# Optimization experiments

Measured on AMD Instinct MI355X. Metric: run time of the kernel, lower is better.

The kernel has to match this reference:

```python
import jax, jax.numpy as jnp
import numpy as np

H = 96
W = 96
FX = 96.0
FY = 96.0
NEAR = 0.3
EPS = 1e-8


def q2r(quat):
    # quat: [N,4] (w,x,y,z) -> [N,3,3]
    q = quat / (jnp.linalg.norm(quat, axis=-1, keepdims=True) + 1e-12)
    w, x, y, z = q[:, 0], q[:, 1], q[:, 2], q[:, 3]
    R = jnp.stack([
        1 - 2 * (y * y + z * z), 2 * (x * y - w * z), 2 * (x * z + w * y),
        2 * (x * y + w * z), 1 - 2 * (x * x + z * z), 2 * (y * z - w * x),
        2 * (x * z - w * y), 2 * (y * z + w * x), 1 - 2 * (x * x + y * y),
    ], axis=-1).reshape(-1, 3, 3)
    return R


def setup_inputs() -> dict:
    key = jax.random.key(0)
    ks = jax.random.split(key, 8)
    N = 4096
    pos_xy = jax.random.uniform(ks[0], (N, 2), minval=-2.0, maxval=2.0, dtype=jnp.float32)
    pos_z = jax.random.uniform(ks[1], (N, 1), minval=2.0, maxval=6.0, dtype=jnp.float32)
    pos = jnp.concatenate([pos_xy, pos_z], axis=-1)
    rgb = jax.random.normal(ks[2], (N, 3), dtype=jnp.float32)
    opa = jax.random.normal(ks[3], (N,), dtype=jnp.float32)
    quat = jax.random.normal(ks[4], (N, 4), dtype=jnp.float32)
    scale = jax.random.uniform(ks[5], (N, 3), dtype=jnp.float32) * 0.05 + 0.005
    rot = jnp.eye(3, dtype=jnp.float32)
    tran = jnp.zeros(3, dtype=jnp.float32)
    return {"pos": pos, "rgb": rgb, "opa": opa, "quat": quat, "scale": scale, "rot": rot, "tran": tran}


def reference(pos, rgb, opa, quat, scale, rot, tran):
    # ---- project: world -> camera -> image space ----
    cam = pos @ rot.T + tran[None, :]              # [N,3]
    x, y, z = cam[:, 0], cam[:, 1], cam[:, 2]
    r = jnp.linalg.norm(cam, axis=-1)              # depth = ray length (camera_to_image)
    mean2d = jnp.stack([x / z, y / z], axis=-1)    # [N,2]

    # jacobian of (x/z, y/z, |p|) wrt camera-space point, [N,3,3]
    zeros = jnp.zeros_like(z)
    J = jnp.stack([
        1.0 / z, zeros, -x / (z * z),
        zeros, 1.0 / z, -y / (z * z),
        x / r, y / r, z / r,
    ], axis=-1).reshape(-1, 3, 3)

    # ---- 3D covariance: R S S^T R^T ----
    R = q2r(quat)                                   # [N,3,3]
    s = jnp.abs(scale) + 1e-4                       # [N,3]
    RS = R * s[:, None, :]                          # R @ diag(s)
    cov3d = jnp.einsum('nij,nkj->nik', RS, RS)      # [N,3,3]

    # ---- 2D covariance: (J W) cov3d (J W)^T, upper-left 2x2 ----
    JW = jnp.einsum('nij,jk->nik', J, rot)          # [N,3,3]
    cov2d = jnp.einsum('nij,njk,nlk->nil', JW, cov3d, JW)[:, :2, :2]  # [N,2,2]

    a = cov2d[:, 0, 0] + EPS
    d = cov2d[:, 1, 1] + EPS
    b = 0.5 * (cov2d[:, 0, 1] + cov2d[:, 1, 0])
    det = a * d - b * b
    inv_a = d / det
    inv_b = -b / det
    inv_d = a / det

    rgb_act = jax.nn.sigmoid(rgb)                   # [N,3]
    opa_act = jax.nn.sigmoid(opa)                   # [N]

    # ---- per-pixel gaussian evaluation in normalized image space ----
    u = (jnp.arange(W, dtype=jnp.float32) + 0.5 - W / 2) / FX   # [W]
    v = (jnp.arange(H, dtype=jnp.float32) + 0.5 - H / 2) / FY   # [H]
    pu = jnp.tile(u, H)                                          # [P]
    pv = jnp.repeat(v, W)                                        # [P]

    dx = pu[None, :] - mean2d[:, 0:1]               # [N,P]
    dy = pv[None, :] - mean2d[:, 1:2]               # [N,P]
    power = -0.5 * (inv_a[:, None] * dx * dx + 2.0 * inv_b[:, None] * dx * dy + inv_d[:, None] * dy * dy)
    alpha = opa_act[:, None] * jnp.exp(power)       # [N,P]
    alpha = jnp.clip(alpha, 0.0, 0.99)
    valid = (z > NEAR).astype(alpha.dtype)[:, None]
    alpha = alpha * valid

    # ---- depth-sorted alpha compositing ----
    order = jnp.argsort(r)                          # near -> far
    alpha_s = alpha[order]                          # [N,P]
    rgb_s = rgb_act[order]                          # [N,3]

    log_1m = jnp.log1p(-alpha_s)                    # [N,P]
    cum = jnp.cumsum(log_1m, axis=0)
    logT = jnp.concatenate([jnp.zeros((1, alpha_s.shape[1]), alpha_s.dtype), cum[:-1]], axis=0)
    w = jnp.exp(logT) * alpha_s                     # [N,P] blending weights
    img = jnp.einsum('np,nc->pc', w, rgb_s)         # [P,3]
    return img.reshape(H, W, 3)
```

## Files before the change

kernel.cpp:

```cpp
#include <hip/hip_runtime.h>
#include <math.h>

#define N_G   4096
#define IMW   96
#define TILE  6
#define TILES_X 16
#define NTILE (TILES_X*TILES_X)
#define NTHR  1024
#define NW    (NTHR/64)
#define NST   (N_G/NTHR)
#define NPX   (TILE*TILE)
#define NSEG  16
#define BCAP  2048
#define CAP   512
#define FXI   (1.0f/96.0f)
#define NEARP 0.3f
#define EPSV  1e-8f
#define LOG2E 1.4426950408889634f
#define LN2   0.6931471805599453f
#define CULL_K 26.0f

typedef unsigned long long ull;

__global__ __launch_bounds__(NTHR, 1) void splat_k(
    const float* __restrict__ pos, const float* __restrict__ rgb,
    const float* __restrict__ opa, const float* __restrict__ quat,
    const float* __restrict__ scale, const float* __restrict__ rot,
    const float* __restrict__ tran, float* __restrict__ out)
{
    __shared__ unsigned int bl[BCAP];
    __shared__ ull skey[CAP];
    __shared__ float4 g0[CAP], g1[CAP], g2[CAP];
    __shared__ float4 pix[NSEG*NPX];
    __shared__ int wsA[NST][NW];
    __shared__ int wsB[NW];

    const int t = threadIdx.x;
    const int tile = blockIdx.x;
    const int tx = tile % TILES_X, ty = tile / TILES_X;
    const float u0 = ((float)(tx*TILE) + 0.5f - 48.0f) * FXI;
    const float u1 = u0 + (TILE-1) * FXI;
    const float v0 = ((float)(ty*TILE) + 0.5f - 48.0f) * FXI;
    const float v1 = v0 + (TILE-1) * FXI;
    const int wid = t >> 6, lane = t & 63;

    float R00=rot[0],R01=rot[1],R02=rot[2];
    float R10=rot[3],R11=rot[4],R12=rot[5];
    float R20=rot[6],R21=rot[7],R22=rot[8];
    float t0=tran[0], t1=tran[1], t2=tran[2];

    float pp0[NST], pp1[NST], pp2[NST], po[NST], ps0[NST], ps1[NST], ps2[NST];
    #pragma unroll
    for (int st = 0; st < NST; st++) {
        int gi = st*NTHR + t;
        pp0[st]=pos[gi*3+0]; pp1[st]=pos[gi*3+1]; pp2[st]=pos[gi*3+2];
        po[st]=opa[gi];
        ps0[st]=scale[gi*3+0]; ps1[st]=scale[gi*3+1]; ps2[st]=scale[gi*3+2];
    }

    int bcnt = 0;
    #pragma unroll
    for (int st = 0; st < NST; st++) {
        int gi = st*NTHR + t;
        float x = R00*pp0[st] + R01*pp1[st] + R02*pp2[st] + t0;
        float y = R10*pp0[st] + R11*pp1[st] + R12*pp2[st] + t1;
        float z = R20*pp0[st] + R21*pp1[st] + R22*pp2[st] + t2;
        float invz = 1.0f/z;
        float mu = x*invz, mv = y*invz;

        float inz2 = invz*invz;
        float fn = 2.0f*inz2 + (x*x + y*y)*inz2*inz2;
        float smax = fmaxf(fmaxf(fabsf(ps0[st]), fabsf(ps1[st])), fabsf(ps2[st])) + 1e-4f;
        float lmax = fn*smax*smax + EPSV;
        float amp = CULL_K + 1.0f + fminf(0.0f, po[st]*LOG2E);
        float r2b = amp * lmax * (2.0f*LN2) * 1.02f;

        float cu = fminf(fmaxf(mu, u0), u1);
        float cv = fminf(fmaxf(mv, v0), v1);
        float ddx = mu - cu, ddy = mv - cv;
        bool flag = (z > NEARP) && (amp > 0.0f) && (ddx*ddx + ddy*ddy <= r2b);

        ull m = __ballot(flag);
        if (lane == 0) wsA[st][wid] = __popcll(m);
        __syncthreads();
        int base = bcnt, tot = 0;
        #pragma unroll
        for (int w = 0; w < NW; w++) { int c = wsA[st][w]; if (w < wid) base += c; tot += c; }
        if (flag) {
            int p = base + __popcll(m & ((1ull << lane) - 1ull));
            if (p < BCAP) bl[p] = (unsigned int)gi;
        }
        bcnt += tot;
    }
    if (bcnt > BCAP) bcnt = BCAP;
    __syncthreads();

    int cnt = 0;
    for (int s0i = 0; s0i < bcnt; s0i += NTHR) {
        int s = s0i + t;
        bool flag = false;
        float4 o0, o1, o2; float rr = 0.0f;
        if (s < bcnt) {
            int gi = bl[s];
            float p0=pos[gi*3+0], p1=pos[gi*3+1], p2=pos[gi*3+2];
            float x = R00*p0 + R01*p1 + R02*p2 + t0;
            float y = R10*p0 + R11*p1 + R12*p2 + t1;
            float z = R20*p0 + R21*p1 + R22*p2 + t2;
            rr = sqrtf(x*x + y*y + z*z);
            float invz = 1.0f/z;
            float mu = x*invz, mv = y*invz;

            float J02 = -x*invz*invz, J12 = -y*invz*invz;
            float JW00 = invz*R00 + J02*R20;
            float JW01 = invz*R01 + J02*R21;
            float JW02 = invz*R02 + J02*R22;
            float JW10 = invz*R10 + J12*R20;
            float JW11 = invz*R11 + J12*R21;
            float JW12 = invz*R12 + J12*R22;

            float qw=quat[gi*4+0], qx=quat[gi*4+1], qy=quat[gi*4+2], qz=quat[gi*4+3];
            float qn = sqrtf(qw*qw+qx*qx+qy*qy+qz*qz) + 1e-12f;
            float qi = 1.0f/qn;
            qw*=qi; qx*=qi; qy*=qi; qz*=qi;
            float Q00=1.f-2.f*(qy*qy+qz*qz), Q01=2.f*(qx*qy-qw*qz), Q02=2.f*(qx*qz+qw*qy);
            float Q10=2.f*(qx*qy+qw*qz), Q11=1.f-2.f*(qx*qx+qz*qz), Q12=2.f*(qy*qz-qw*qx);
            float Q20=2.f*(qx*qz-qw*qy), Q21=2.f*(qy*qz+qw*qx), Q22=1.f-2.f*(qx*qx+qy*qy);

            float sa=fabsf(scale[gi*3+0])+1e-4f;
            float sb=fabsf(scale[gi*3+1])+1e-4f;
            float sc=fabsf(scale[gi*3+2])+1e-4f;
            float A00=Q00*sa,A01=Q01*sb,A02=Q02*sc;
            float A10=Q10*sa,A11=Q11*sb,A12=Q12*sc;
            float A20=Q20*sa,A21=Q21*sb,A22=Q22*sc;
            float C00=A00*A00+A01*A01+A02*A02;
            float C01=A00*A10+A01*A11+A02*A12;
            float C02=A00*A20+A01*A21+A02*A22;
            float C11=A10*A10+A11*A11+A12*A12;
            float C12=A10*A20+A11*A21+A12*A22;
            float C22=A20*A20+A21*A21+A22*A22;
            float M00=JW00*C00+JW01*C01+JW02*C02;
            float M01=JW00*C01+JW01*C11+JW02*C12;
            float M02=JW00*C02+JW01*C12+JW02*C22;
            float M10=JW10*C00+JW11*C01+JW12*C02;
            float M11=JW10*C01+JW11*C11+JW12*C12;
            float M12=JW10*C02+JW11*C12+JW12*C22;
            float a  = M00*JW00+M01*JW01+M02*JW02 + EPSV;
            float d  = M10*JW10+M11*JW11+M12*JW12 + EPSV;
            float bb = 0.5f*((M00*JW10+M01*JW11+M02*JW12)+(M10*JW00+M11*JW01+M12*JW02));
            float invdet = 1.0f/(a*d - bb*bb);
            float iaP = -0.5f*d*invdet*LOG2E;
            float ibP =  bb*invdet*LOG2E;
            float idP = -0.5f*a*invdet*LOG2E;

            float sig_o = 1.0f/(1.0f+__expf(-opa[gi]));
            float opa_eff = (z > NEARP) ? sig_o : 0.0f;

            float q00 = -iaP, q01 = -0.5f*ibP, q11 = -idP;
            float df = q00 - q11;
            float lam = 0.5f*((q00 + q11) - sqrtf(df*df + 4.0f*q01*q01));
            lam = fmaxf(lam, 1e-20f);
            float r2 = (CULL_K + log2f(opa_eff)) / lam;

            float cu = fminf(fmaxf(mu, u0), u1);
            float cv = fminf(fmaxf(mv, v0), v1);
            float ddx = mu - cu, ddy = mv - cv;
            flag = (ddx*ddx + ddy*ddy) <= r2;

            if (flag) {
                float c0 = 1.0f/(1.0f+__expf(-rgb[gi*3+0]));
                float c1 = 1.0f/(1.0f+__expf(-rgb[gi*3+1]));
                float c2 = 1.0f/(1.0f+__expf(-rgb[gi*3+2]));
                o0 = make_float4(mu, mv, iaP, ibP);
                o1 = make_float4(idP, opa_eff, c0, c1);
                o2 = make_float4(c2, 0.0f, 0.0f, 0.0f);
            }
        }
        ull m = __ballot(flag);
        if (lane == 0) wsB[wid] = __popcll(m);
        __syncthreads();
        int base = cnt, tot = 0;
        #pragma unroll
        for (int w = 0; w < NW; w++) { int c = wsB[w]; if (w < wid) base += c; tot += c; }
        if (flag) {
            int p = base + __popcll(m & ((1ull << lane) - 1ull));
            if (p < CAP) {
                g0[p] = o0; g1[p] = o1; g2[p] = o2;
                skey[p] = ((ull)__float_as_uint(rr) << 32) | (unsigned int)p;
            }
        }
        cnt += tot;
        __syncthreads();
    }
    if (cnt > CAP) cnt = CAP;

    ull v = 0; int r = -1;
    if (t < cnt) {
        v = skey[t];
        r = 0;
        for (int j = 0; j < cnt; j++) r += (skey[j] < v) ? 1 : 0;
    }
    __syncthreads();
    if (r >= 0) skey[r] = v;
    __syncthreads();

    if (t < NSEG*NPX) {
        const int seg = t / NPX, pid = t % NPX;
        const int px = tx*TILE + (pid % TILE);
        const int py = ty*TILE + (pid / TILE);
        const float pu = ((float)px + 0.5f - 48.0f) * FXI;
        const float pv = ((float)py + 0.5f - 48.0f) * FXI;

        const int per = (cnt + NSEG - 1) / NSEG;
        const int sA = min(seg * per, cnt);
        const int sB = min(sA + per, cnt);

        float T = 1.0f, cr = 0.0f, cg = 0.0f, cb = 0.0f;
        for (int s = sA; s < sB; s++) {
            int slot = (int)(skey[s] & 0xffffffffu);
            float4 a0 = g0[slot];
            float4 a1 = g1[slot];
            float4 a2 = g2[slot];
            float dx = pu - a0.x;
            float dy = pv - a0.y;
            float pw = dx*(a0.z*dx + a0.w*dy) + a1.x*dy*dy;
            float al = fminf(a1.y * __builtin_amdgcn_exp2f(pw), 0.99f);
            float w = T * al;
            cr += w * a1.z;
            cg += w * a1.w;
            cb += w * a2.x;
            T *= (1.0f - al);
        }
        pix[t] = make_float4(cr, cg, cb, T);
    }
    __syncthreads();

    if (t < NPX) {
        float orr = 0.0f, og = 0.0f, ob = 0.0f, T2 = 1.0f;
        #pragma unroll
        for (int s = 0; s < NSEG; s++) {
            float4 P = pix[s*NPX + t];
            orr += T2 * P.x;
            og  += T2 * P.y;
            ob  += T2 * P.z;
            T2  *= P.w;
        }
        int px = tx*TILE + (t % TILE);
        int py = ty*TILE + (t / TILE);
        int pixel = py * IMW + px;
        out[pixel*3+0] = orr;
        out[pixel*3+1] = og;
        out[pixel*3+2] = ob;
    }
}

extern "C" void kernel_launch(void* const* d_in, const int* in_sizes, int n_in,
                              void* d_out, int out_size, void* d_ws, size_t ws_size,
                              hipStream_t stream) {
    const float* pos   = (const float*)d_in[0];
    const float* rgb   = (const float*)d_in[1];
    const float* opa   = (const float*)d_in[2];
    const float* quat  = (const float*)d_in[3];
    const float* scale = (const float*)d_in[4];
    const float* rot   = (const float*)d_in[5];
    const float* tran  = (const float*)d_in[6];
    float* out = (float*)d_out;

    splat_k<<<NTILE, NTHR, 0, stream>>>(pos, rgb, opa, quat, scale, rot, tran, out);
}
```

Baseline: 14.94 us.

## Stash projected gaussians in LDS and split rank-sort across two thread halves

The first culling pass now stores each gaussian's projected mean, depth, effective opacity and ray length in shared memory. The second pass reads these back instead of reloading positions and recomputing the projection, and it loads the quaternion as one float4. The rank sort is split so two 512-thread groups each count half of the keys using 128-bit vector loads, and the partial ranks are summed afterwards. The blue channel moves to a scalar array and BCAP shrinks, at the cost of about 80KB of extra LDS and a sigmoid plus log2 for every gaussian in the first pass.

New measurement: 15.76 us. +5.5%, slower.

```diff
diff --git a/kernel.cpp b/kernel.cpp
--- a/kernel.cpp
+++ b/kernel.cpp
@@ -11,7 +11,7 @@
 #define NST   (N_G/NTHR)
 #define NPX   (TILE*TILE)
 #define NSEG  16
-#define BCAP  2048
+#define BCAP  1536
 #define CAP   512
 #define FXI   (1.0f/96.0f)
 #define NEARP 0.3f
@@ -21,6 +21,7 @@
 #define CULL_K 26.0f
 
 typedef unsigned long long ull;
+typedef __attribute__((ext_vector_type(2))) unsigned long long ull2;
 
 __global__ __launch_bounds__(NTHR, 1) void splat_k(
     const float* __restrict__ pos, const float* __restrict__ rgb,
@@ -29,11 +30,15 @@
     const float* __restrict__ tran, float* __restrict__ out)
 {
     __shared__ unsigned int bl[BCAP];
-    __shared__ ull skey[CAP];
-    __shared__ float4 g0[CAP], g1[CAP], g2[CAP];
+    __shared__ __align__(16) ull skey[CAP+4];
+    __shared__ float4 g0[CAP], g1[CAP];
+    __shared__ float  g2[CAP];
     __shared__ float4 pix[NSEG*NPX];
     __shared__ int wsA[NST][NW];
     __shared__ int wsB[NW];
+    __shared__ int psum[2][CAP];
+    __shared__ float4 stash[N_G];
+    __shared__ float  rrs[N_G];
 
     const int t = threadIdx.x;
     const int tile = blockIdx.x;
@@ -65,20 +70,26 @@
         float x = R00*pp0[st] + R01*pp1[st] + R02*pp2[st] + t0;
         float y = R10*pp0[st] + R11*pp1[st] + R12*pp2[st] + t1;
         float z = R20*pp0[st] + R21*pp1[st] + R22*pp2[st] + t2;
+        float rr = sqrtf(x*x + y*y + z*z);
         float invz = 1.0f/z;
         float mu = x*invz, mv = y*invz;
+
+        float sig_o = 1.0f/(1.0f+__expf(-po[st]));
+        float opa_eff = (z > NEARP) ? sig_o : 0.0f;
+        stash[gi] = make_float4(mu, mv, z, opa_eff);
+        rrs[gi] = rr;
 
         float inz2 = invz*invz;
         float fn = 2.0f*inz2 + (x*x + y*y)*inz2*inz2;
         float smax = fmaxf(fmaxf(fabsf(ps0[st]), fabsf(ps1[st])), fabsf(ps2[st])) + 1e-4f;
         float lmax = fn*smax*smax + EPSV;
-        float amp = CULL_K + 1.0f + fminf(0.0f, po[st]*LOG2E);
+        float amp = CULL_K + 1.0f + log2f(opa_eff);
         float r2b = amp * lmax * (2.0f*LN2) * 1.02f;
 
         float cu = fminf(fmaxf(mu, u0), u1);
         float cv = fminf(fmaxf(mv, v0), v1);
         float ddx = mu - cu, ddy = mv - cv;
-        bool flag = (z > NEARP) && (amp > 0.0f) && (ddx*ddx + ddy*ddy <= r2b);
+        bool flag = (amp > 0.0f) && (ddx*ddx + ddy*ddy <= r2b);
 
         ull m = __ballot(flag);
         if (lane == 0) wsA[st][wid] = __popcll(m);
@@ -99,18 +110,15 @@
     for (int s0i = 0; s0i < bcnt; s0i += NTHR) {
         int s = s0i + t;
         bool flag = false;
-        float4 o0, o1, o2; float rr = 0.0f;
+        float4 o0, o1; float ocb = 0.0f, rr = 0.0f;
         if (s < bcnt) {
             int gi = bl[s];
-            float p0=pos[gi*3+0], p1=pos[gi*3+1], p2=pos[gi*3+2];
-            float x = R00*p0 + R01*p1 + R02*p2 + t0;
-            float y = R10*p0 + R11*p1 + R12*p2 + t1;
-            float z = R20*p0 + R21*p1 + R22*p2 + t2;
-            rr = sqrtf(x*x + y*y + z*z);
+            float4 sg = stash[gi];
+            rr = rrs[gi];
+            float mu = sg.x, mv = sg.y, z = sg.z, opa_eff = sg.w;
             float invz = 1.0f/z;
-            float mu = x*invz, mv = y*invz;
-
-            float J02 = -x*invz*invz, J12 = -y*invz*invz;
+
+            float J02 = -mu*invz, J12 = -mv*invz;
             float JW00 = invz*R00 + J02*R20;
             float JW01 = invz*R01 + J02*R21;
             float JW02 = invz*R02 + J02*R22;
@@ -118,7 +126,8 @@
             float JW11 = invz*R11 + J12*R21;
             float JW12 = invz*R12 + J12*R22;
 
-            float qw=quat[gi*4+0], qx=quat[gi*4+1], qy=quat[gi*4+2], qz=quat[gi*4+3];
+            const float4 qv = ((const float4*)quat)[gi];
+            float qw=qv.x, qx=qv.y, qy=qv.z, qz=qv.w;
             float qn = sqrtf(qw*qw+qx*qx+qy*qy+qz*qz) + 1e-12f;
             float qi = 1.0f/qn;
             qw*=qi; qx*=qi; qy*=qi; qz*=qi;
@@ -152,9 +161,6 @@
             float ibP =  bb*invdet*LOG2E;
             float idP = -0.5f*a*invdet*LOG2E;
 
-            float sig_o = 1.0f/(1.0f+__expf(-opa[gi]));
-            float opa_eff = (z > NEARP) ? sig_o : 0.0f;
-
             float q00 = -iaP, q01 = -0.5f*ibP, q11 = -idP;
             float df = q00 - q11;
             float lam = 0.5f*((q00 + q11) - sqrtf(df*df + 4.0f*q01*q01));
@@ -172,7 +178,7 @@
                 float c2 = 1.0f/(1.0f+__expf(-rgb[gi*3+2]));
                 o0 = make_float4(mu, mv, iaP, ibP);
                 o1 = make_float4(idP, opa_eff, c0, c1);
-                o2 = make_float4(c2, 0.0f, 0.0f, 0.0f);
+                ocb = c2;
             }
         }
         ull m = __ballot(flag);
@@ -184,7 +190,7 @@
         if (flag) {
             int p = base + __popcll(m & ((1ull << lane) - 1ull));
             if (p < CAP) {
-                g0[p] = o0; g1[p] = o1; g2[p] = o2;
+                g0[p] = o0; g1[p] = o1; g2[p] = ocb;
                 skey[p] = ((ull)__float_as_uint(rr) << 32) | (unsigned int)p;
             }
         }
@@ -193,14 +199,31 @@
     }
     if (cnt > CAP) cnt = CAP;
 
-    ull v = 0; int r = -1;
+    int cnt2 = cnt + (cnt & 1);
+    if (t == 0 && (cnt & 1)) skey[cnt] = ~0ull;
+    __syncthreads();
+    int h = ((cnt2 >> 1) + 1) & ~1;
+    if (h > cnt2) h = cnt2;
+    const int g = t >> 9, e = t & 511;
+    ull v = 0;
+    if (e < cnt) {
+        v = skey[e];
+        const ull2* sk2 = (const ull2*)skey;
+        int wA2 = g ? (h >> 1) : 0;
+        int wB2 = g ? (cnt2 >> 1) : (h >> 1);
+        int c = 0;
+        for (int w = wA2; w < wB2; w++) {
+            ull2 p = sk2[w];
+            c += (p.x < v) ? 1 : 0;
+            c += (p.y < v) ? 1 : 0;
+        }
+        psum[g][e] = c;
+    }
+    __syncthreads();
     if (t < cnt) {
-        v = skey[t];
-        r = 0;
-        for (int j = 0; j < cnt; j++) r += (skey[j] < v) ? 1 : 0;
-    }
-    __syncthreads();
-    if (r >= 0) skey[r] = v;
+        int r = psum[0][t] + psum[1][t];
+        skey[r] = v;
+    }
     __syncthreads();
 
     if (t < NSEG*NPX) {
@@ -219,7 +242,7 @@
             int slot = (int)(skey[s] & 0xffffffffu);
             float4 a0 = g0[slot];
             float4 a1 = g1[slot];
-            float4 a2 = g2[slot];
+            float a2 = g2[slot];
             float dx = pu - a0.x;
             float dy = pv - a0.y;
             float pw = dx*(a0.z*dx + a0.w*dy) + a1.x*dy*dy;
@@ -227,7 +250,7 @@
             float w = T * al;
             cr += w * a1.z;
             cg += w * a1.w;
-            cb += w * a2.x;
+            cb += w * a2;
             T *= (1.0f - al);
         }
         pix[t] = make_float4(cr, cg, cb, T);
```
